# Performance work log

Measured on AMD Instinct MI355X. Metric: run time of the kernel, lower is better.

## Reference

```python
import jax, jax.numpy as jnp
import numpy as np

N, E = 100000, 1200000
IN_NF, H_NF, OUT_NF, IN_EF = 32, 64, 64, 16


def _linear_params(key, fan_in, fan_out):
    kw, kb = jax.random.split(key)
    s = 1.0 / np.sqrt(fan_in)
    W = jax.random.uniform(kw, (fan_in, fan_out), jnp.float32, -s, s)
    b = jax.random.uniform(kb, (fan_out,), jnp.float32, -s, s)
    return W, b


def setup_inputs() -> dict:
    key = jax.random.key(0)
    ks = jax.random.split(key, 16)
    inp = {
        'node_feats': jax.random.normal(ks[0], (N, IN_NF), jnp.float32),
        'edge_attr': jax.random.normal(ks[1], (E, IN_EF), jnp.float32),
        'coords': jax.random.normal(ks[2], (N, 3), jnp.float32),
        'edge_index': jax.random.randint(ks[3], (2, E), 0, N, jnp.int64),
    }
    # emb_in / emb_out
    inp['W_in'], inp['b_in'] = _linear_params(ks[4], IN_NF, H_NF)
    inp['W_out'], inp['b_out'] = _linear_params(ks[5], H_NF, OUT_NF)
    # edge MLP: cat[h_i, h_j, radial, edge_attr] -> hidden -> hidden
    edge_in = 2 * H_NF + 1 + IN_EF
    inp['We1'], inp['be1'] = _linear_params(ks[6], edge_in, H_NF)
    inp['We2'], inp['be2'] = _linear_params(ks[7], H_NF, H_NF)
    # node MLP: cat[h, agg_m] -> hidden -> out
    inp['Wn1'], inp['bn1'] = _linear_params(ks[8], H_NF + H_NF, H_NF)
    inp['Wn2'], inp['bn2'] = _linear_params(ks[9], H_NF, H_NF)
    # coord MLP: m -> hidden -> 1
    inp['Wc1'], inp['bc1'] = _linear_params(ks[10], H_NF, H_NF)
    inp['Wc2'], inp['bc2'] = _linear_params(ks[11], H_NF, 1)
    return inp


def _egnn_fwd(node_feats, edge_attr, coords, edge_index,
              W_in, b_in, We1, be1, We2, be2, Wn1, bn1, Wn2, bn2,
              Wc1, bc1, Wc2, bc2, W_out, b_out):
    relu = jax.nn.relu
    n = node_feats.shape[0]
    row, col = edge_index[0], edge_index[1]

    h = node_feats @ W_in + b_in                       # [N, H]

    # --- edge model ---
    coord_diff = coords[row] - coords[col]             # [E, 3]
    radial = jnp.sum(coord_diff * coord_diff, axis=-1, keepdims=True)  # [E, 1]
    edge_in = jnp.concatenate([h[row], h[col], radial, edge_attr], axis=-1)
    m = relu(relu(edge_in @ We1 + be1) @ We2 + be2)    # [E, H]

    # --- coord model: mean-aggregate coord_diff * phi_x(m) ---
    trans = coord_diff * (relu(m @ Wc1 + bc1) @ Wc2 + bc2)  # [E, 3]
    agg_x = jax.ops.segment_sum(trans, row, num_segments=n)
    cnt = jax.ops.segment_sum(jnp.ones((trans.shape[0],), trans.dtype), row, num_segments=n)
    coords = coords + agg_x / jnp.maximum(cnt, 1.0)[:, None]

    # --- node model: sum-aggregate messages ---
    agg_m = jax.ops.segment_sum(m, row, num_segments=n)  # [N, H]
    h = relu(jnp.concatenate([h, agg_m], axis=-1) @ Wn1 + bn1) @ Wn2 + bn2

    out = h @ W_out + b_out                            # [N, OUT]
    return out, coords


def reference(node_feats, edge_attr, coords, edge_index,
              W_in, b_in, W_out, b_out, We1, be1, We2, be2,
              Wn1, bn1, Wn2, bn2, Wc1, bc1, Wc2, bc2):
    return _egnn_fwd(node_feats, edge_attr, coords, edge_index,
                     W_in, b_in, We1, be1, We2, be2, Wn1, bn1, Wn2, bn2,
                     Wc1, bc1, Wc2, bc2, W_out, b_out)
```

## Files before the change

### kernel.cpp

```cpp
#include <hip/hip_runtime.h>
#include <hip/hip_bf16.h>


typedef __attribute__((ext_vector_type(4))) float f32x4;
typedef __attribute__((ext_vector_type(8))) short short8;

__device__ __forceinline__ void atomAddF(float* p, float v) { unsafeAtomicAdd(p, v); }

__device__ __forceinline__ unsigned int pack2bf(float lo, float hi) {
  unsigned int r;
  asm("v_cvt_pk_bf16_f32 %0, %1, %2" : "=v"(r) : "v"(lo), "v"(hi));
  return r;
}
__device__ __forceinline__ unsigned short f2bf(float f) {
  return (unsigned short)(pack2bf(f, 0.f) & 0xFFFFu);
}
__device__ __forceinline__ float bf2f(unsigned short s) {
  unsigned int v = ((unsigned int)s) << 16;
  return __builtin_bit_cast(float, v);
}
__device__ __forceinline__ float lo_bf(unsigned int u) {
  return __builtin_bit_cast(float, u << 16);
}
__device__ __forceinline__ float hi_bf(unsigned int u) {
  return __builtin_bit_cast(float, u & 0xFFFF0000u);
}

__global__ __launch_bounds__(256) void k_prep(
    const float* __restrict__ nf, const float* __restrict__ W_in,
    const float* __restrict__ b_in, const float* __restrict__ We1,
    const float* __restrict__ be1, const float* __restrict__ Wn1,
    const float* __restrict__ bn1, const float* __restrict__ Wn2,
    const float* __restrict__ bn2, const float* __restrict__ W_out,
    const float* __restrict__ b_out, unsigned short* __restrict__ nfb,
    float* __restrict__ WA, float* __restrict__ WB, float* __restrict__ WF1,
    float* __restrict__ Wno, float* __restrict__ bSum, float* __restrict__ bn1f,
    float* __restrict__ bno, float* __restrict__ aggz, int N) {
  const int b = blockIdx.x, t = threadIdx.x;
  if (b == 0 || b == 1) {
    const float* Wsrc = (b == 0) ? We1 : (We1 + 64 * 64);
    float* dst = (b == 0) ? WA : WB;
    for (int idx = t; idx < 2048; idx += 256) {
      const int i = idx >> 6, n = idx & 63;
      float s = 0.f;
      for (int h = 0; h < 64; ++h) s = fmaf(W_in[i * 64 + h], Wsrc[h * 64 + n], s);
      dst[idx] = s;
    }
  } else if (b == 2) {
    for (int idx = t; idx < 2048; idx += 256) {
      const int i = idx >> 6, n = idx & 63;
      float s = 0.f;
      for (int h = 0; h < 64; ++h) s = fmaf(W_in[i * 64 + h], Wn1[h * 64 + n], s);
      WF1[idx] = s;
    }
    if (t < 64) {
      float s1 = bn1[t], s2 = be1[t];
      for (int h = 0; h < 64; ++h) {
        s1 = fmaf(b_in[h], Wn1[h * 64 + t], s1);
        s2 = fmaf(b_in[h], We1[h * 64 + t] + We1[(64 + h) * 64 + t], s2);
      }
      bn1f[t] = s1;
      bSum[t] = s2;
    }
  } else if (b <= 6) {
    const int base = (b - 3) * 1024;
    for (int idx = t; idx < 1024; idx += 256) {
      const int kk = (base + idx) >> 6, n = (base + idx) & 63;
      float s = 0.f;
      for (int h = 0; h < 64; ++h) s = fmaf(Wn2[kk * 64 + h], W_out[h * 64 + n], s);
      Wno[base + idx] = s;
    }
    if (b == 3 && t < 64) {
      float s = b_out[t];
      for (int h = 0; h < 64; ++h) s = fmaf(bn2[h], W_out[h * 64 + t], s);
      bno[t] = s;
    }
  } else {
    const int bid = b - 7, nb = gridDim.x - 7;
    const int tot8 = N * 8;
    for (int i = bid * 256 + t; i < tot8; i += nb * 256) {
      const f32x4 v = *reinterpret_cast<const f32x4*>(nf + (size_t)i * 4);
      uint2 o;
      o.x = pack2bf(v[0], v[1]);
      o.y = pack2bf(v[2], v[3]);
      *reinterpret_cast<uint2*>(nfb + (size_t)i * 4) = o;
    }
    const size_t tot = (size_t)N * 68;
    for (size_t i = (size_t)bid * 256 + t; i * 4 < tot; i += (size_t)nb * 256) {
      const size_t off = i * 4;
      if (off + 4 <= tot)
        *reinterpret_cast<float4*>(aggz + off) = make_float4(0.f, 0.f, 0.f, 0.f);
      else
        for (size_t q = off; q < tot; ++q) aggz[q] = 0.f;
    }
  }
}

__global__ __launch_bounds__(256) void k_gab(
    const float* __restrict__ nf, const float* __restrict__ WA,
    const float* __restrict__ WB, unsigned short* __restrict__ gA,
    unsigned short* __restrict__ gB, int N) {
  __shared__ float Ws[2 * 2048];
  __shared__ float nfl[4][8][36];
  for (int i = threadIdx.x; i < 2048; i += 256) {
    Ws[i] = WA[i];
    Ws[2048 + i] = WB[i];
  }
  __syncthreads();
  const int w = threadIdx.x >> 6, lane = threadIdx.x & 63;
  const int NG = (N + 7) >> 3;
  for (int ng = blockIdx.x * 4 + w; ng < NG; ng += gridDim.x * 4) {
    const int base = ng * 8;
    {
      const int nl = lane >> 3, ch = lane & 7;
      int n = base + nl;
      if (n >= N) n = N - 1;
      const f32x4 v = *reinterpret_cast<const f32x4*>(nf + (size_t)n * 32 + ch * 4);
      *reinterpret_cast<f32x4*>(&nfl[w][nl][ch * 4]) = v;
    }
    float aa[8], ab[8];
#pragma unroll
    for (int i = 0; i < 8; ++i) { aa[i] = 0.f; ab[i] = 0.f; }
    for (int k4 = 0; k4 < 8; ++k4) {
      float w0[2][4];
#pragma unroll
      for (int q = 0; q < 4; ++q) {
        w0[0][q] = Ws[(k4 * 4 + q) * 64 + lane];
        w0[1][q] = Ws[2048 + (k4 * 4 + q) * 64 + lane];
      }
#pragma unroll
      for (int i = 0; i < 8; ++i) {
        const f32x4 x = *reinterpret_cast<const f32x4*>(&nfl[w][i][k4 * 4]);
#pragma unroll
        for (int q = 0; q < 4; ++q) {
          aa[i] = fmaf(x[q], w0[0][q], aa[i]);
          ab[i] = fmaf(x[q], w0[1][q], ab[i]);
        }
      }
    }
#pragma unroll
    for (int i = 0; i < 8; ++i) {
      const int n = base + i;
      if (n < N) {
        gA[(size_t)n * 64 + lane] = f2bf(aa[i]);
        gB[(size_t)n * 64 + lane] = f2bf(ab[i]);
      }
    }
  }
}

__global__ __launch_bounds__(256) void k_hist(const int* __restrict__ eidx,
                                              int* __restrict__ deg, int E) {
  for (int e = blockIdx.x * 256 + threadIdx.x; e < E; e += gridDim.x * 256)
    atomicAdd(&deg[eidx[e]], 1);
}

__global__ __launch_bounds__(256) void k_scanA(const int* __restrict__ deg,
                                               int* __restrict__ excl,
                                               int* __restrict__ bsum, int N) {
  __shared__ int s[256];
  const int t = threadIdx.x;
  const int i = blockIdx.x * 256 + t;
  const int v = (i < N) ? deg[i] : 0;
  s[t] = v;
  __syncthreads();
#pragma unroll
  for (int off = 1; off < 256; off <<= 1) {
    int x = 0;
    if (t >= off) x = s[t - off];
    __syncthreads();
    s[t] += x;
    __syncthreads();
  }
  if (i < N) excl[i] = s[t] - v;
  if (t == 255) bsum[blockIdx.x] = s[255];
}

__global__ __launch_bounds__(256) void k_scanC(int* __restrict__ excl,
                                               const int* __restrict__ bsum,
                                               int N) {
  __shared__ int sh[256];
  const int t = threadIdx.x, b = blockIdx.x;
  int part = 0;
  for (int i = t; i < b; i += 256) part += bsum[i];
  sh[t] = part;
  __syncthreads();
#pragma unroll
  for (int off = 128; off; off >>= 1) {
    if (t < off) sh[t] += sh[t + off];
    __syncthreads();
  }
  const int add = sh[0];
  const int i = b * 256 + t;
  if (i < N) excl[i] += add;
}

__global__ __launch_bounds__(256) void k_scatter(
    const int* __restrict__ eidx, int* __restrict__ rowNext,
    unsigned long long* __restrict__ srt8, int E) {
  for (int e = blockIdx.x * 256 + threadIdx.x; e < E; e += gridDim.x * 256) {
    const int r = eidx[e];
    const int c = eidx[E + e];
    const int pos = atomicAdd(&rowNext[r], 1);
    srt8[pos] = (unsigned long long)r | ((unsigned long long)c << 18) |
                ((unsigned long long)e << 36);
  }
}

struct EdgeLds {
  unsigned short We2t[64 * 72];
  unsigned short Wc1t[64 * 72];
  unsigned short Bea[64 * 40];
  unsigned short x[4][16 * 72];
  float cd[4][16 * 4];
  int idx[4][16];
};

__global__ __launch_bounds__(256, 3) void k_edge(
    const unsigned short* __restrict__ gA, const unsigned short* __restrict__ gB,
    const float* __restrict__ ea, const float* __restrict__ co,
    const unsigned long long* __restrict__ srt8, const float* __restrict__ We1,
    const float* __restrict__ bSum, const float* __restrict__ be2,
    const float* __restrict__ We2, const float* __restrict__ bc1,
    const float* __restrict__ Wc1, const float* __restrict__ Wc2,
    const float* __restrict__ bc2, float* __restrict__ agg_m,
    float* __restrict__ agg_x, int E) {
  __shared__ EdgeLds S;
  const int tid = threadIdx.x;
  for (int i = tid; i < 4096; i += 256) {
    const int k = i >> 6, n = i & 63;
    S.We2t[n * 72 + k] = f2bf(We2[k * 64 + n]);
    S.Wc1t[n * 72 + k] = f2bf(Wc1[k * 64 + n]);
  }
  for (int i = tid; i < 2048; i += 256) {
    const int k = i >> 6, n = i & 63;
    const float v = (k < 16) ? We1[(129 + k) * 64 + n]
                             : ((k == 16) ? We1[128 * 64 + n] : 0.f);
    S.Bea[n * 40 + k] = f2bf(v);
  }
  __syncthreads();

  const int w = tid >> 6, lane = tid & 63;
  const int g = lane >> 4, t = lane & 15;
  const float bc2v = bc2[0];

  float bS_r[4], be2_r[4], bc1_r[4], wc2_r[4];
#pragma unroll
  for (int nt = 0; nt < 4; ++nt) {
    const int n = t + 16 * nt;
    bS_r[nt] = bSum[n];
    be2_r[nt] = be2[n];
    bc1_r[nt] = bc1[n];
    wc2_r[nt] = Wc2[n];
  }

  unsigned short* xw = &S.x[w][0];
  float* cdw = &S.cd[w][0];
  int* idxw = &S.idx[w][0];
  const int ngroups = (E + 15) >> 4;
  const int GS = gridDim.x * 4;

  for (int grp = blockIdx.x * 4 + w; grp < ngroups; grp += GS) {
    const int e0 = grp * 16;
    unsigned long long s8 = 0;
    if (lane < 16) {
      int e = e0 + lane;
      if (e >= E) e = E - 1;
      s8 = srt8[e];
    }
    const int r_dec = (int)(s8 & 0x3FFFFull);
    const int c_dec = (int)((s8 >> 18) & 0x3FFFFull);
    const int p_dec = (int)(s8 >> 36);
    if (lane < 16) {
      idxw[lane] = r_dec;
      const float dx = co[(size_t)r_dec * 3 + 0] - co[(size_t)c_dec * 3 + 0];
      const float dy = co[(size_t)r_dec * 3 + 1] - co[(size_t)c_dec * 3 + 1];
      const float dz = co[(size_t)r_dec * 3 + 2] - co[(size_t)c_dec * 3 + 2];
      f32x4 c4;
      c4[0] = dx; c4[1] = dy; c4[2] = dz; c4[3] = dx * dx + dy * dy + dz * dz;
      *reinterpret_cast<f32x4*>(&cdw[lane * 4]) = c4;
    }

#pragma unroll
    for (int rr = 0; rr < 2; ++rr) {
      const int el = rr * 8 + (lane >> 3), ch = lane & 7;
      const int rI = __shfl(r_dec, el, 64);
      const int cI = __shfl(c_dec, el, 64);
      const uint4 va = *reinterpret_cast<const uint4*>(gA + (size_t)rI * 64 + ch * 8);
      const uint4 vb = *reinterpret_cast<const uint4*>(gB + (size_t)cI * 64 + ch * 8);
      const unsigned int a[4] = {va.x, va.y, va.z, va.w};
      const unsigned int b[4] = {vb.x, vb.y, vb.z, vb.w};
      uint4 o;
      unsigned int r[4];
#pragma unroll
      for (int q = 0; q < 4; ++q) {
        const float s0 = lo_bf(a[q]) + lo_bf(b[q]);
        const float s1 = hi_bf(a[q]) + hi_bf(b[q]);
        r[q] = pack2bf(s0, s1);
      }
      o.x = r[0]; o.y = r[1]; o.z = r[2]; o.w = r[3];
      *reinterpret_cast<uint4*>(&xw[el * 72 + ch * 8]) = o;
    }

    short8 a1;
    {
      const int eaI = __shfl(p_dec, t, 64);
      short8 a = {};
      if (g < 2) {
        const float* pe2 = ea + (size_t)eaI * 16 + g * 8;
        const f32x4 x0 = *reinterpret_cast<const f32x4*>(pe2);
        const f32x4 x1 = *reinterpret_cast<const f32x4*>(pe2 + 4);
        const unsigned int p0 = pack2bf(x0[0], x0[1]);
        const unsigned int p1 = pack2bf(x0[2], x0[3]);
        const unsigned int p2 = pack2bf(x1[0], x1[1]);
        const unsigned int p3 = pack2bf(x1[2], x1[3]);
        a[0] = (short)(p0 & 0xFFFF); a[1] = (short)(p0 >> 16);
        a[2] = (short)(p1 & 0xFFFF); a[3] = (short)(p1 >> 16);
        a[4] = (short)(p2 & 0xFFFF); a[5] = (short)(p2 >> 16);
        a[6] = (short)(p3 & 0xFFFF); a[7] = (short)(p3 >> 16);
      } else if (g == 2) {
        a[0] = (short)f2bf(cdw[t * 4 + 3]);
      }
      a1 = a;
    }

    f32x4 acc[4];
#pragma unroll
    for (int nt = 0; nt < 4; ++nt)
#pragma unroll
      for (int j = 0; j < 4; ++j) {
        const int row = g * 4 + j, col = t + 16 * nt;
        acc[nt][j] = bf2f(xw[row * 72 + col]) + bS_r[nt];
      }
#pragma unroll
    for (int nt = 0; nt < 4; ++nt) {
      const short8 b = *reinterpret_cast<const short8*>(&S.Bea[(t + 16 * nt) * 40 + g * 8]);
      acc[nt] = __builtin_amdgcn_mfma_f32_16x16x32_bf16(a1, b, acc[nt], 0, 0, 0);
    }
#pragma unroll
    for (int nt = 0; nt < 4; ++nt) {
      const unsigned int pk01 = pack2bf(fmaxf(acc[nt][0], 0.f), fmaxf(acc[nt][1], 0.f));
      const unsigned int pk23 = pack2bf(fmaxf(acc[nt][2], 0.f), fmaxf(acc[nt][3], 0.f));
      xw[(g * 4 + 0) * 72 + t + 16 * nt] = (unsigned short)(pk01 & 0xFFFF);
      xw[(g * 4 + 1) * 72 + t + 16 * nt] = (unsigned short)(pk01 >> 16);
      xw[(g * 4 + 2) * 72 + t + 16 * nt] = (unsigned short)(pk23 & 0xFFFF);
      xw[(g * 4 + 3) * 72 + t + 16 * nt] = (unsigned short)(pk23 >> 16);
    }
    short8 A2[2];
#pragma unroll
    for (int kt = 0; kt < 2; ++kt)
      A2[kt] = *reinterpret_cast<const short8*>(&xw[t * 72 + kt * 32 + g * 8]);
    f32x4 m2[4];
#pragma unroll
    for (int nt = 0; nt < 4; ++nt) {
      f32x4 c;
      c[0] = be2_r[nt]; c[1] = be2_r[nt]; c[2] = be2_r[nt]; c[3] = be2_r[nt];
#pragma unroll
      for (int kt = 0; kt < 2; ++kt) {
        const short8 b = *reinterpret_cast<const short8*>(
            &S.We2t[(t + 16 * nt) * 72 + kt * 32 + g * 8]);
        c = __builtin_amdgcn_mfma_f32_16x16x32_bf16(A2[kt], b, c, 0, 0, 0);
      }
#pragma unroll
      for (int j = 0; j < 4; ++j) c[j] = fmaxf(c[j], 0.f);
      m2[nt] = c;
    }
#pragma unroll
    for (int nt = 0; nt < 4; ++nt) {
      const unsigned int pk01 = pack2bf(m2[nt][0], m2[nt][1]);
      const unsigned int pk23 = pack2bf(m2[nt][2], m2[nt][3]);
      xw[(g * 4 + 0) * 72 + t + 16 * nt] = (unsigned short)(pk01 & 0xFFFF);
      xw[(g * 4 + 1) * 72 + t + 16 * nt] = (unsigned short)(pk01 >> 16);
      xw[(g * 4 + 2) * 72 + t + 16 * nt] = (unsigned short)(pk23 & 0xFFFF);
      xw[(g * 4 + 3) * 72 + t + 16 * nt] = (unsigned short)(pk23 >> 16);
    }

    short8 A3[2];
#pragma unroll
    for (int kt = 0; kt < 2; ++kt)
      A3[kt] = *reinterpret_cast<const short8*>(&xw[t * 72 + kt * 32 + g * 8]);
    float sv[4];
#pragma unroll
    for (int j = 0; j < 4; ++j) sv[j] = 0.f;
#pragma unroll
    for (int nt = 0; nt < 4; ++nt) {
      f32x4 c;
      c[0] = bc1_r[nt]; c[1] = bc1_r[nt]; c[2] = bc1_r[nt]; c[3] = bc1_r[nt];
#pragma unroll
      for (int kt = 0; kt < 2; ++kt) {
        const short8 b = *reinterpret_cast<const short8*>(
            &S.Wc1t[(t + 16 * nt) * 72 + kt * 32 + g * 8]);
        c = __builtin_amdgcn_mfma_f32_16x16x32_bf16(A3[kt], b, c, 0, 0, 0);
      }
#pragma unroll
      for (int j = 0; j < 4; ++j) sv[j] = fmaf(fmaxf(c[j], 0.f), wc2_r[nt], sv[j]);
    }
#pragma unroll
    for (int d = 1; d < 16; d <<= 1)
#pragma unroll
      for (int j = 0; j < 4; ++j) sv[j] += __shfl_xor(sv[j], d, 64);
#pragma unroll
    for (int j = 0; j < 4; ++j) sv[j] += bc2v;
#pragma unroll
    for (int j = 0; j < 4; ++j)
      if (t == 0) cdw[(g * 4 + j) * 4 + 3] = sv[j];

    {
      float accm = 0.f;
#pragma unroll
      for (int r = 0; r < 16; ++r) {
        const int rIr = idxw[r];
        const bool valid = (e0 + r) < E;
        if (valid) accm += bf2f(xw[r * 72 + lane]);
        const bool closes = (r == 15) || ((e0 + r + 1) >= E) || (idxw[r + 1] != rIr);
        if (valid && closes) {
          atomAddF(&agg_m[(size_t)rIr * 64 + lane], accm);
          accm = 0.f;
        }
      }
    }
    if (lane < 3) {
      float accx = 0.f;
#pragma unroll
      for (int r = 0; r < 16; ++r) {
        const int rIr = idxw[r];
        const bool valid = (e0 + r) < E;
        if (valid) accx += cdw[r * 4 + lane] * cdw[r * 4 + 3];
        const bool closes = (r == 15) || ((e0 + r + 1) >= E) || (idxw[r + 1] != rIr);
        if (valid && closes) {
          atomAddF(&agg_x[(size_t)rIr * 3 + lane], accx);
          accx = 0.f;
        }
      }
    }
  }
}

struct NodeLds {
  unsigned short Wn1bT[64 * 72];
  unsigned short WnoT[64 * 72];
  unsigned short x[4][32 * 72];
};

__global__ __launch_bounds__(256, 4) void k_node(
    const unsigned short* __restrict__ nfb, const float* __restrict__ agg_m,
    const float* __restrict__ agg_x, const int* __restrict__ deg,
    const float* __restrict__ co, const float* __restrict__ WF1,
    const float* __restrict__ Wn1, const float* __restrict__ Wno,
    const float* __restrict__ bn1f, const float* __restrict__ bno,
    float* __restrict__ out, float* __restrict__ co_out, int N) {
  __shared__ NodeLds S;
  const int tid = threadIdx.x;
  for (int i = tid; i < 4096; i += 256) {
    const int k = i >> 6, n = i & 63;
    S.Wn1bT[n * 72 + k] = f2bf(Wn1[(64 + k) * 64 + n]);
    S.WnoT[n * 72 + k] = f2bf(Wno[k * 64 + n]);
  }
  __syncthreads();
  const int w = tid >> 6, lane = tid & 63;
  const int g = lane >> 4, t = lane & 15;

  short8 fW1[4];
  float b1_r[4], bo_r[4];
#pragma unroll
  for (int nt = 0; nt < 4; ++nt) {
    const int n = t + 16 * nt;
    short8 a;
#pragma unroll
    for (int j = 0; j < 8; ++j) a[j] = (short)f2bf(WF1[(g * 8 + j) * 64 + n]);
    fW1[nt] = a;
    b1_r[nt] = bn1f[n];
    bo_r[nt] = bno[n];
  }

  unsigned short* xw = &S.x[w][0];
  const int ngroups = (N + 31) >> 5;
  const int GS = gridDim.x * 4;

  for (int grp = blockIdx.x * 4 + w; grp < ngroups; grp += GS) {
    const int base = grp * 32;
    short8 A1[2], Aa[2][2];
#pragma unroll
    for (int mt = 0; mt < 2; ++mt) {
      int node = base + t + 16 * mt;
      if (node >= N) node = N - 1;
      A1[mt] = *reinterpret_cast<const short8*>(nfb + (size_t)node * 32 + g * 8);
#pragma unroll
      for (int kt = 0; kt < 2; ++kt) {
        const f32x4 v0 = *reinterpret_cast<const f32x4*>(
            agg_m + (size_t)node * 64 + kt * 32 + g * 8);
        const f32x4 v1 = *reinterpret_cast<const f32x4*>(
            agg_m + (size_t)node * 64 + kt * 32 + g * 8 + 4);
        const unsigned int p0 = pack2bf(v0[0], v0[1]);
        const unsigned int p1 = pack2bf(v0[2], v0[3]);
        const unsigned int p2 = pack2bf(v1[0], v1[1]);
        const unsigned int p3 = pack2bf(v1[2], v1[3]);
        short8 a;
        a[0] = (short)(p0 & 0xFFFF); a[1] = (short)(p0 >> 16);
        a[2] = (short)(p1 & 0xFFFF); a[3] = (short)(p1 >> 16);
        a[4] = (short)(p2 & 0xFFFF); a[5] = (short)(p2 >> 16);
        a[6] = (short)(p3 & 0xFFFF); a[7] = (short)(p3 >> 16);
        Aa[mt][kt] = a;
      }
    }
    f32x4 acc[2][4];
#pragma unroll
    for (int mt = 0; mt < 2; ++mt)
#pragma unroll
      for (int nt = 0; nt < 4; ++nt) {
        const int n = t + 16 * nt;
        f32x4 c;
        c[0] = b1_r[nt]; c[1] = b1_r[nt]; c[2] = b1_r[nt]; c[3] = b1_r[nt];
        c = __builtin_amdgcn_mfma_f32_16x16x32_bf16(A1[mt], fW1[nt], c, 0, 0, 0);
#pragma unroll
        for (int kt = 0; kt < 2; ++kt) {
          const short8 b = *reinterpret_cast<const short8*>(
              &S.Wn1bT[n * 72 + kt * 32 + g * 8]);
          c = __builtin_amdgcn_mfma_f32_16x16x32_bf16(Aa[mt][kt], b, c, 0, 0, 0);
        }
        acc[mt][nt] = c;
      }
#pragma unroll
    for (int mt = 0; mt < 2; ++mt)
#pragma unroll
      for (int nt = 0; nt < 4; ++nt)
#pragma unroll
        for (int j = 0; j < 4; ++j)
          xw[(g * 4 + j + 16 * mt) * 72 + t + 16 * nt] =
              f2bf(fmaxf(acc[mt][nt][j], 0.f));
    short8 A2[2][2];
#pragma unroll
    for (int mt = 0; mt < 2; ++mt)
#pragma unroll
      for (int kt = 0; kt < 2; ++kt)
        A2[mt][kt] = *reinterpret_cast<const short8*>(
            &S.x[w][(t + 16 * mt) * 72 + kt * 32 + g * 8]);
#pragma unroll
    for (int mt = 0; mt < 2; ++mt)
#pragma unroll
      for (int nt = 0; nt < 4; ++nt) {
        const int n = t + 16 * nt;
        f32x4 c;
        c[0] = bo_r[nt]; c[1] = bo_r[nt]; c[2] = bo_r[nt]; c[3] = bo_r[nt];
#pragma unroll
        for (int kt = 0; kt < 2; ++kt) {
          const short8 b = *reinterpret_cast<const short8*>(
              &S.WnoT[n * 72 + kt * 32 + g * 8]);
          c = __builtin_amdgcn_mfma_f32_16x16x32_bf16(A2[mt][kt], b, c, 0, 0, 0);
        }
#pragma unroll
        for (int j = 0; j < 4; ++j) {
          const int node = base + g * 4 + j + 16 * mt;
          if (node < N) out[(size_t)node * 64 + n] = c[j];
        }
      }
    if (lane < 32) {
      const int node = base + lane;
      if (node < N) {
        const float dv = fmaxf((float)deg[node], 1.f);
#pragma unroll
        for (int d = 0; d < 3; ++d)
          co_out[(size_t)node * 3 + d] =
              co[(size_t)node * 3 + d] + agg_x[(size_t)node * 3 + d] / dv;
      }
    }
  }
}

extern "C" void kernel_launch(void* const* d_in, const int* in_sizes, int n_in,
                              void* d_out, int out_size, void* d_ws, size_t ws_size,
                              hipStream_t stream) {
  const float* nf = (const float*)d_in[0];
  const float* ea = (const float*)d_in[1];
  const float* co = (const float*)d_in[2];
  const int* ei = (const int*)d_in[3];
  const float* W_in = (const float*)d_in[4];
  const float* b_in = (const float*)d_in[5];
  const float* W_out = (const float*)d_in[6];
  const float* b_out = (const float*)d_in[7];
  const float* We1 = (const float*)d_in[8];
  const float* be1 = (const float*)d_in[9];
  const float* We2 = (const float*)d_in[10];
  const float* be2 = (const float*)d_in[11];
  const float* Wn1 = (const float*)d_in[12];
  const float* bn1 = (const float*)d_in[13];
  const float* Wn2 = (const float*)d_in[14];
  const float* bn2 = (const float*)d_in[15];
  const float* Wc1 = (const float*)d_in[16];
  const float* bc1 = (const float*)d_in[17];
  const float* Wc2 = (const float*)d_in[18];
  const float* bc2 = (const float*)d_in[19];

  const int N = in_sizes[0] / 32;
  const int E = in_sizes[1] / 16;

  float* ws = (float*)d_ws;
  float* agg_m = ws;
  float* agg_x = agg_m + (size_t)N * 64;
  int* deg = (int*)(agg_x + (size_t)N * 3);
  float* WA = (float*)(deg + N);
  float* WB = WA + 2048;
  float* WF1 = WB + 2048;
  float* Wno = WF1 + 2048;
  float* bSum = Wno + 4096;
  float* bn1f = bSum + 64;
  float* bno = bn1f + 64;
  int* rowNext = (int*)(bno + 64);
  int* bsumBuf = rowNext + N;
  uintptr_t pp = (uintptr_t)(bsumBuf + 512);
  pp = (pp + 7) & ~(uintptr_t)7;
  unsigned long long* srt8 = (unsigned long long*)pp;
  unsigned short* nfb = (unsigned short*)(srt8 + E);

  float* outp = (float*)d_out;
  float* co_out = outp + (size_t)N * 64;
  unsigned short* gA = (unsigned short*)d_out;
  unsigned short* gB = gA + (size_t)N * 64;

  const int nb = (N + 255) / 256;

  k_prep<<<1031, 256, 0, stream>>>(nf, W_in, b_in, We1, be1, Wn1, bn1, Wn2,
                                   bn2, W_out, b_out, nfb, WA, WB, WF1, Wno,
                                   bSum, bn1f, bno, agg_m, N);
  k_gab<<<2048, 256, 0, stream>>>(nf, WA, WB, gA, gB, N);
  k_hist<<<512, 256, 0, stream>>>(ei, deg, E);
  k_scanA<<<nb, 256, 0, stream>>>(deg, rowNext, bsumBuf, N);
  k_scanC<<<nb, 256, 0, stream>>>(rowNext, bsumBuf, N);
  k_scatter<<<512, 256, 0, stream>>>(ei, rowNext, srt8, E);
  k_edge<<<1024, 256, 0, stream>>>(gA, gB, ea, co, srt8, We1, bSum, be2, We2,
                                   bc1, Wc1, Wc2, bc2, agg_m, agg_x, E);
  k_node<<<1024, 256, 0, stream>>>(nfb, agg_m, agg_x, deg, co, WF1, Wn1, Wno,
                                   bn1f, bno, outp, co_out, N);
}
```

Baseline: 435.8 us.

## Merge histogram into gab kernel and precompute coord diffs during scatter

Folds the degree histogram into the k_gab launch as extra blocks, which removes one kernel launch and lets the two run at the same time. The coordinate difference and radial computation moves from k_edge into k_scatter, which writes a sorted f32x4 per edge so k_edge does one coalesced load instead of random coordinate gathers. The scatter grid doubles. In exchange this adds a 16-byte-per-edge workspace buffer that must be written and read back, plus extra random coordinate reads inside scatter.

```diff
diff --git a/kernel.cpp b/kernel.cpp
--- a/kernel.cpp
+++ b/kernel.cpp
@@ -99,7 +99,15 @@
 __global__ __launch_bounds__(256) void k_gab(
     const float* __restrict__ nf, const float* __restrict__ WA,
     const float* __restrict__ WB, unsigned short* __restrict__ gA,
-    unsigned short* __restrict__ gB, int N) {
+    unsigned short* __restrict__ gB, const int* __restrict__ eidx,
+    int* __restrict__ deg, int N, int E, int gabBlocks) {
+  if ((int)blockIdx.x >= gabBlocks) {
+    const int hb = blockIdx.x - gabBlocks;
+    const int nhb = gridDim.x - gabBlocks;
+    for (int e = hb * 256 + threadIdx.x; e < E; e += nhb * 256)
+      atomicAdd(&deg[eidx[e]], 1);
+    return;
+  }
   __shared__ float Ws[2 * 2048];
   __shared__ float nfl[4][8][36];
   for (int i = threadIdx.x; i < 2048; i += 256) {
@@ -109,7 +117,7 @@
   __syncthreads();
   const int w = threadIdx.x >> 6, lane = threadIdx.x & 63;
   const int NG = (N + 7) >> 3;
-  for (int ng = blockIdx.x * 4 + w; ng < NG; ng += gridDim.x * 4) {
+  for (int ng = blockIdx.x * 4 + w; ng < NG; ng += gabBlocks * 4) {
     const int base = ng * 8;
     {
       const int nl = lane >> 3, ch = lane & 7;
@@ -147,12 +155,6 @@
       }
     }
   }
-}
-
-__global__ __launch_bounds__(256) void k_hist(const int* __restrict__ eidx,
-                                              int* __restrict__ deg, int E) {
-  for (int e = blockIdx.x * 256 + threadIdx.x; e < E; e += gridDim.x * 256)
-    atomicAdd(&deg[eidx[e]], 1);
 }
 
 __global__ __launch_bounds__(256) void k_scanA(const int* __restrict__ deg,
@@ -196,14 +198,21 @@
 }
 
 __global__ __launch_bounds__(256) void k_scatter(
-    const int* __restrict__ eidx, int* __restrict__ rowNext,
-    unsigned long long* __restrict__ srt8, int E) {
+    const int* __restrict__ eidx, const float* __restrict__ co,
+    int* __restrict__ rowNext, unsigned long long* __restrict__ srt8,
+    f32x4* __restrict__ cdr, int E) {
   for (int e = blockIdx.x * 256 + threadIdx.x; e < E; e += gridDim.x * 256) {
     const int r = eidx[e];
     const int c = eidx[E + e];
     const int pos = atomicAdd(&rowNext[r], 1);
     srt8[pos] = (unsigned long long)r | ((unsigned long long)c << 18) |
                 ((unsigned long long)e << 36);
+    const float dx = co[(size_t)r * 3 + 0] - co[(size_t)c * 3 + 0];
+    const float dy = co[(size_t)r * 3 + 1] - co[(size_t)c * 3 + 1];
+    const float dz = co[(size_t)r * 3 + 2] - co[(size_t)c * 3 + 2];
+    f32x4 c4;
+    c4[0] = dx; c4[1] = dy; c4[2] = dz; c4[3] = dx * dx + dy * dy + dz * dz;
+    cdr[pos] = c4;
   }
 }
 
@@ -218,7 +227,7 @@
 
 __global__ __launch_bounds__(256, 3) void k_edge(
     const unsigned short* __restrict__ gA, const unsigned short* __restrict__ gB,
-    const float* __restrict__ ea, const float* __restrict__ co,
+    const float* __restrict__ ea, const f32x4* __restrict__ cdr,
     const unsigned long long* __restrict__ srt8, const float* __restrict__ We1,
     const float* __restrict__ bSum, const float* __restrict__ be2,
     const float* __restrict__ We2, const float* __restrict__ bc1,
@@ -267,19 +276,12 @@
       int e = e0 + lane;
       if (e >= E) e = E - 1;
       s8 = srt8[e];
+      *reinterpret_cast<f32x4*>(&cdw[lane * 4]) = cdr[e];
     }
     const int r_dec = (int)(s8 & 0x3FFFFull);
     const int c_dec = (int)((s8 >> 18) & 0x3FFFFull);
     const int p_dec = (int)(s8 >> 36);
-    if (lane < 16) {
-      idxw[lane] = r_dec;
-      const float dx = co[(size_t)r_dec * 3 + 0] - co[(size_t)c_dec * 3 + 0];
-      const float dy = co[(size_t)r_dec * 3 + 1] - co[(size_t)c_dec * 3 + 1];
-      const float dz = co[(size_t)r_dec * 3 + 2] - co[(size_t)c_dec * 3 + 2];
-      f32x4 c4;
-      c4[0] = dx; c4[1] = dy; c4[2] = dz; c4[3] = dx * dx + dy * dy + dz * dz;
-      *reinterpret_cast<f32x4*>(&cdw[lane * 4]) = c4;
-    }
+    if (lane < 16) idxw[lane] = r_dec;
 
 #pragma unroll
     for (int rr = 0; rr < 2; ++rr) {
@@ -608,8 +610,9 @@
   int* rowNext = (int*)(bno + 64);
   int* bsumBuf = rowNext + N;
   uintptr_t pp = (uintptr_t)(bsumBuf + 512);
-  pp = (pp + 7) & ~(uintptr_t)7;
-  unsigned long long* srt8 = (unsigned long long*)pp;
+  pp = (pp + 15) & ~(uintptr_t)15;
+  f32x4* cdr = (f32x4*)pp;
+  unsigned long long* srt8 = (unsigned long long*)(cdr + E);
   unsigned short* nfb = (unsigned short*)(srt8 + E);
 
   float* outp = (float*)d_out;
@@ -622,12 +625,11 @@
   k_prep<<<1031, 256, 0, stream>>>(nf, W_in, b_in, We1, be1, Wn1, bn1, Wn2,
                                    bn2, W_out, b_out, nfb, WA, WB, WF1, Wno,
                                    bSum, bn1f, bno, agg_m, N);
-  k_gab<<<2048, 256, 0, stream>>>(nf, WA, WB, gA, gB, N);
-  k_hist<<<512, 256, 0, stream>>>(ei, deg, E);
+  k_gab<<<2048 + 512, 256, 0, stream>>>(nf, WA, WB, gA, gB, ei, deg, N, E, 2048);
   k_scanA<<<nb, 256, 0, stream>>>(deg, rowNext, bsumBuf, N);
   k_scanC<<<nb, 256, 0, stream>>>(rowNext, bsumBuf, N);
-  k_scatter<<<512, 256, 0, stream>>>(ei, rowNext, srt8, E);
-  k_edge<<<1024, 256, 0, stream>>>(gA, gB, ea, co, srt8, We1, bSum, be2, We2,
+  k_scatter<<<1024, 256, 0, stream>>>(ei, co, rowNext, srt8, cdr, E);
+  k_edge<<<1024, 256, 0, stream>>>(gA, gB, ea, cdr, srt8, We1, bSum, be2, We2,
                                    bc1, Wc1, Wc2, bc2, agg_m, agg_x, E);
   k_node<<<1024, 256, 0, stream>>>(nfb, agg_m, agg_x, deg, co, WF1, Wn1, Wno,
                                    bn1f, bno, outp, co_out, N);
```

Result: faster. 390.7 us (-10.3%).
